# Kernel optimization log

Measured on AMD Instinct MI355X. Metric: run time of the kernel, lower is better.

Reference implementation:

```python
import jax, jax.numpy as jnp
import numpy as np

S, B, H = 2048, 2, 2048
NH = 16
HD = H // NH
SCALE = HD ** -0.5


def setup_inputs() -> dict:
    key = jax.random.key(0)
    ks = jax.random.split(key, 5)
    sigma = 0.02
    return {
        "x": jax.random.normal(ks[0], (S, B, H), dtype=jnp.float32),
        "wq": jax.random.normal(ks[1], (H, H), dtype=jnp.float32) * sigma,
        "wk": jax.random.normal(ks[2], (H, H), dtype=jnp.float32) * sigma,
        "wv": jax.random.normal(ks[3], (H, H), dtype=jnp.float32) * sigma,
        "wo": jax.random.normal(ks[4], (H, H), dtype=jnp.float32) * sigma,
    }


def reference(x, wq, wk, wv, wo):
    # x: [s, b, h]; F.linear(x, W) == x @ W.T
    q = x @ wq.T
    k = x @ wk.T
    v = x @ wv.T
    s, b, _ = q.shape
    # [s, b, h] -> [b, nh, s, hd]
    def split_heads(t):
        return t.reshape(s, b, NH, HD).transpose(1, 2, 0, 3)
    q, k, v = split_heads(q), split_heads(k), split_heads(v)
    scores = jnp.einsum("bhqd,bhkd->bhqk", q, k) * SCALE
    attn = jax.nn.softmax(scores.astype(jnp.float32), axis=-1).astype(q.dtype)
    out = jnp.einsum("bhqk,bhkd->bhqd", attn, v)
    # [b, nh, s, hd] -> [s, b, h]
    out = out.transpose(2, 0, 1, 3).reshape(s, b, NH * HD)
    return out @ wo.T
```

## Files before the change

### kernel.cpp

```cpp
#include <hip/hip_runtime.h>

typedef __bf16 bf16;
typedef __bf16 bf16x8 __attribute__((ext_vector_type(8)));
typedef float f32x4 __attribute__((ext_vector_type(4)));
typedef float f32x16 __attribute__((ext_vector_type(16)));
typedef unsigned int uint;
typedef uint uint2v __attribute__((ext_vector_type(2)));

#define GLOAD16(g, l)                                                        \
  __builtin_amdgcn_global_load_lds(                                          \
      (const __attribute__((address_space(1))) void*)(g),                    \
      (__attribute__((address_space(3))) void*)(l), 16, 0, 0)

__device__ inline uint pack_bf16(float a, float b) {
  union { bf16 h[2]; uint u; } x;
  x.h[0] = (bf16)a; x.h[1] = (bf16)b;
  return x.u;
}

__global__ void cast_f32_to_bf16(const float* __restrict__ in,
                                 bf16* __restrict__ out, int n8, float scale) {
  int i = blockIdx.x * blockDim.x + threadIdx.x;
  if (i >= n8) return;
  const float4* p = reinterpret_cast<const float4*>(in) + (size_t)i * 2;
  float4 a = p[0], b = p[1];
  bf16x8 o;
  o[0] = (bf16)(a.x * scale); o[1] = (bf16)(a.y * scale);
  o[2] = (bf16)(a.z * scale); o[3] = (bf16)(a.w * scale);
  o[4] = (bf16)(b.x * scale); o[5] = (bf16)(b.y * scale);
  o[6] = (bf16)(b.z * scale); o[7] = (bf16)(b.w * scale);
  *reinterpret_cast<bf16x8*>(out + (size_t)i * 8) = o;
}

template <typename OT>
__global__ __launch_bounds__(512, 2) void gemm_nt_256(
    const bf16* __restrict__ A, const bf16* __restrict__ B, OT* __restrict__ C,
    int K, int lda, int ldb, int ldc, long bsB, long bsC, long cSplit) {
  extern __shared__ char sh[];
  const int t = threadIdx.x;
  const int w = t >> 6, lane = t & 63;
  const int l15 = lane & 15, l4 = lane >> 4;
  const int wr = w >> 1, wc = w & 1;
  const int gx = gridDim.x, gy = gridDim.y;
  const int nwg = gx * gy;
  const int bid = blockIdx.y * gx + blockIdx.x;
  const int fid = (bid & 7) * (nwg >> 3) + (bid >> 3);
  const int by = fid / gx, bx = fid - by * gx;
  const int m0 = by * 256;
  const int n0 = bx * 128;
  const bf16* Bg = B + (size_t)blockIdx.z * bsB;
  OT* Cg = C + (size_t)blockIdx.z * bsC + ((n0 & 2048) ? cSplit : 0);

  int sRow[4], sCol[4];
#pragma unroll
  for (int i = 0; i < 4; i++) {
    int sB_ = (i * 512 + t) * 16;
    int row = sB_ >> 7;
    int ge = (sB_ ^ ((row & 7) << 4)) >> 1;
    sRow[i] = ge >> 6;
    sCol[i] = ge & 63;
  }

  const int NT = K >> 6;
  f32x4 acc[4][4] = {};

  auto stage = [&](int tt) {
    char* dst = sh + (size_t)(tt % 3) * 49152;
    const int k0 = tt * 64;
#pragma unroll
    for (int i = 0; i < 4; i++)
      GLOAD16(A + (size_t)(m0 + sRow[i]) * lda + k0 + sCol[i],
              dst + (i * 512 + w * 64) * 16);
#pragma unroll
    for (int i = 0; i < 2; i++)
      GLOAD16(Bg + (size_t)(n0 + sRow[i]) * ldb + k0 + sCol[i],
              dst + 32768 + (i * 512 + w * 64) * 16);
  };

  stage(0);
  stage(1);
  for (int tt = 0; tt < NT; ++tt) {
    if (tt < NT - 1)
      asm volatile("s_waitcnt vmcnt(6)" ::: "memory");
    else
      asm volatile("s_waitcnt vmcnt(0)" ::: "memory");
    __builtin_amdgcn_s_barrier();

    const char* Ab = sh + (size_t)(tt % 3) * 49152;
    const char* Bb = Ab + 32768;
    bf16x8 bfr[4][2];
#pragma unroll
    for (int n = 0; n < 4; n++)
#pragma unroll
      for (int kk = 0; kk < 2; kk++) {
        int row = wc * 64 + n * 16 + l15;
        int off = (row * 128 + kk * 64 + l4 * 16) ^ ((row & 7) << 4);
        bfr[n][kk] = *reinterpret_cast<const bf16x8*>(Bb + off);
      }
    bf16x8 af0[2][2];
#pragma unroll
    for (int m = 0; m < 2; m++)
#pragma unroll
      for (int kk = 0; kk < 2; kk++) {
        int row = wr * 64 + m * 16 + l15;
        int off = (row * 128 + kk * 64 + l4 * 16) ^ ((row & 7) << 4);
        af0[m][kk] = *reinterpret_cast<const bf16x8*>(Ab + off);
      }
    __builtin_amdgcn_s_setprio(1);
#pragma unroll
    for (int m = 0; m < 2; m++)
#pragma unroll
      for (int n = 0; n < 4; n++)
#pragma unroll
        for (int kk = 0; kk < 2; kk++)
          acc[m][n] = __builtin_amdgcn_mfma_f32_16x16x32_bf16(
              af0[m][kk], bfr[n][kk], acc[m][n], 0, 0, 0);
    __builtin_amdgcn_s_setprio(0);

    if (tt + 2 < NT) stage(tt + 2);

    bf16x8 af1[2][2];
#pragma unroll
    for (int m = 0; m < 2; m++)
#pragma unroll
      for (int kk = 0; kk < 2; kk++) {
        int row = wr * 64 + (2 + m) * 16 + l15;
        int off = (row * 128 + kk * 64 + l4 * 16) ^ ((row & 7) << 4);
        af1[m][kk] = *reinterpret_cast<const bf16x8*>(Ab + off);
      }
    __builtin_amdgcn_s_setprio(1);
#pragma unroll
    for (int m = 0; m < 2; m++)
#pragma unroll
      for (int n = 0; n < 4; n++)
#pragma unroll
        for (int kk = 0; kk < 2; kk++)
          acc[2 + m][n] = __builtin_amdgcn_mfma_f32_16x16x32_bf16(
              af1[m][kk], bfr[n][kk], acc[2 + m][n], 0, 0, 0);
    __builtin_amdgcn_s_setprio(0);
  }

#pragma unroll
  for (int m = 0; m < 4; m++)
#pragma unroll
    for (int n = 0; n < 4; n++)
#pragma unroll
      for (int j = 0; j < 4; j++) {
        int row = m0 + wr * 64 + m * 16 + l4 * 4 + j;
        int col = n0 + wc * 64 + n * 16 + l15;
        Cg[(size_t)row * ldc + col] = (OT)acc[m][n][j];
      }
}

__global__ __launch_bounds__(512, 2) void attn_fwd(
    const bf16* __restrict__ Q, const bf16* __restrict__ Kb,
    const bf16* __restrict__ Vt, bf16* __restrict__ O) {
  extern __shared__ char ash[];
  const int t = threadIdx.x, w = t >> 6, lane = t & 63;
  const int l31 = lane & 31, half = lane >> 5;
  const int bh = blockIdx.x;
  const int b = bh >> 4, h = bh & 15;
  const int sq0 = blockIdx.y * 256 + w * 32;
  const size_t hoff = (size_t)h * 128;
  const size_t bO = (size_t)b * 2048 + hoff;

  bf16x8 qf[8];
  {
    const bf16* qp = Q + ((size_t)(sq0 + l31) * 2 + b) * 2048 + hoff + half * 8;
#pragma unroll
    for (int dc = 0; dc < 8; dc++)
      qf[dc] = *reinterpret_cast<const bf16x8*>(qp + dc * 16);
  }

  const bf16* kp[2];
  const bf16* vp[2];
#pragma unroll
  for (int i = 0; i < 2; i++) {
    int s = i * 512 + t;
    int row = s >> 4, g = s & 15;
    int lg = g ^ (row & 15);
    kp[i] = Kb + ((size_t)row * 2 + b) * 2048 + hoff + lg * 8;
    int d = row * 2 + (lg >> 3);
    vp[i] = Vt + (bO + d) * 2048 + (lg & 7) * 8;
  }

  auto stage = [&](int slot, int sk0) {
    char* Kd = ash + (size_t)slot * 32768;
    char* Vd = Kd + 16384;
#pragma unroll
    for (int i = 0; i < 2; i++)
      GLOAD16(kp[i] + (size_t)sk0 * 4096, Kd + (i * 512 + w * 64) * 16);
#pragma unroll
    for (int i = 0; i < 2; i++)
      GLOAD16(vp[i] + sk0, Vd + (i * 512 + w * 64) * 16);
  };

  f32x16 acc_o[4] = {};
  float m_run = -3e38f, l_run = 0.f;

  stage(0, 0);
  stage(1, 64);

  for (int it = 0; it < 32; ++it) {
    if (it < 31)
      asm volatile("s_waitcnt vmcnt(4)" ::: "memory");
    else
      asm volatile("s_waitcnt vmcnt(0)" ::: "memory");
    __builtin_amdgcn_s_barrier();

    const char* ksb = ash + (size_t)(it % 3) * 32768;
    const char* vsb = ksb + 16384;

    f32x16 sc[2] = {};
    __builtin_amdgcn_s_setprio(1);
#pragma unroll
    for (int dc = 0; dc < 8; dc++) {
      int kx = ((dc * 2 + half) ^ (l31 & 15)) << 4;
#pragma unroll
      for (int kt = 0; kt < 2; kt++) {
        int kB = ((kt * 32 + l31) << 8) + kx;
        bf16x8 kf = *reinterpret_cast<const bf16x8*>(ksb + kB);
        sc[kt] = __builtin_amdgcn_mfma_f32_32x32x16_bf16(kf, qf[dc], sc[kt], 0, 0, 0);
      }
    }
    __builtin_amdgcn_s_setprio(0);

    if (it + 2 < 32) stage((it + 2) % 3, (it + 2) * 64);

    float red[8];
#pragma unroll
    for (int r = 0; r < 8; r++)
      red[r] = fmaxf(fmaxf(sc[0][r], sc[0][r + 8]),
                     fmaxf(sc[1][r], sc[1][r + 8]));
#pragma unroll
    for (int s = 4; s >= 1; s >>= 1)
#pragma unroll
      for (int r = 0; r < s; r++) red[r] = fmaxf(red[r], red[r + s]);
    float pmax = fmaxf(red[0], __shfl_xor(red[0], 32));

    if (!__all(pmax - m_run <= 11.0f)) {
      float mn = fmaxf(m_run, pmax);
      float f = exp2f(m_run - mn);
      m_run = mn;
      l_run *= f;
#pragma unroll
      for (int idx = 0; idx < 16; idx++) {
        float fr = __shfl(f, (idx & 3) + 8 * (idx >> 2) + half * 4);
#pragma unroll
        for (int dcb = 0; dcb < 4; dcb++) acc_o[dcb][idx] *= fr;
      }
    }

#pragma unroll
    for (int kt = 0; kt < 2; kt++)
#pragma unroll
      for (int r = 0; r < 16; r++) sc[kt][r] = exp2f(sc[kt][r] - m_run);
#pragma unroll
    for (int r = 0; r < 8; r++)
      red[r] = (sc[0][r] + sc[0][r + 8]) + (sc[1][r] + sc[1][r + 8]);
#pragma unroll
    for (int s = 4; s >= 1; s >>= 1)
#pragma unroll
      for (int r = 0; r < s; r++) red[r] += red[r + s];
    l_run += red[0] + __shfl_xor(red[0], 32);

    uint pa[4][4];
#pragma unroll
    for (int skc = 0; skc < 4; skc++) {
      int kt = skc >> 1, s8 = (skc & 1) * 8;
      uint pk01 = pack_bf16(sc[kt][s8 + 0], sc[kt][s8 + 1]);
      uint pk23 = pack_bf16(sc[kt][s8 + 2], sc[kt][s8 + 3]);
      uint pk45 = pack_bf16(sc[kt][s8 + 4], sc[kt][s8 + 5]);
      uint pk67 = pack_bf16(sc[kt][s8 + 6], sc[kt][s8 + 7]);
      uint2v r02 = __builtin_amdgcn_permlane32_swap(pk01, pk45, false, false);
      uint2v r13 = __builtin_amdgcn_permlane32_swap(pk23, pk67, false, false);
      pa[skc][0] = r02[0];
      pa[skc][1] = r13[0];
      pa[skc][2] = r02[1];
      pa[skc][3] = r13[1];
    }

    __builtin_amdgcn_s_setprio(1);
#pragma unroll
    for (int dcb = 0; dcb < 4; dcb++) {
      int rp = dcb * 16 + (l31 >> 1);
      int pbit = (l31 & 1) << 3;
#pragma unroll
      for (int skc = 0; skc < 4; skc++) {
        int vB = (rp << 8) + (((pbit + skc * 2 + half) ^ (l31 >> 1)) << 4);
        bf16x8 vf = *reinterpret_cast<const bf16x8*>(vsb + vB);
        union { uint u[4]; bf16x8 v; } af;
        af.u[0] = pa[skc][0]; af.u[1] = pa[skc][1];
        af.u[2] = pa[skc][2]; af.u[3] = pa[skc][3];
        acc_o[dcb] = __builtin_amdgcn_mfma_f32_32x32x16_bf16(
            af.v, vf, acc_o[dcb], 0, 0, 0);
      }
    }
    __builtin_amdgcn_s_setprio(0);
  }

  float inv = 1.0f / l_run;
#pragma unroll
  for (int idx = 0; idx < 16; idx++) {
    int sr = (idx & 3) + 8 * (idx >> 2) + half * 4;
    float invr = __shfl(inv, sr);
    bf16* op = O + ((size_t)(sq0 + sr) * 2 + b) * 2048 + hoff + l31;
#pragma unroll
    for (int dcb = 0; dcb < 4; dcb++)
      op[dcb * 32] = (bf16)(acc_o[dcb][idx] * invr);
  }
}

extern "C" void kernel_launch(void* const* d_in, const int* in_sizes, int n_in,
                              void* d_out, int out_size, void* d_ws,
                              size_t ws_size, hipStream_t stream) {
  (void)in_sizes; (void)n_in; (void)out_size; (void)ws_size;
  const float* x  = (const float*)d_in[0];
  const float* wq = (const float*)d_in[1];
  const float* wk = (const float*)d_in[2];
  const float* wv = (const float*)d_in[3];
  const float* wo = (const float*)d_in[4];
  float* out = (float*)d_out;
  char* ws = (char*)d_ws;
  bf16* xb   = (bf16*)(ws);
  bf16* qb   = (bf16*)(ws + (1u << 24));
  bf16* kb   = (bf16*)(ws + (2u << 24));
  bf16* vt   = (bf16*)(ws + (3u << 24));
  bf16* wb   = (bf16*)(ws + (4u << 24));
  bf16* wqk  = vt;
  bf16* attn = xb;
  const float SCALE = 0.08838834764831845f * 1.4426950408889634f;
  const int SMEM = 3 * 49152;
  const int SMEM_A = 3 * 32768;
  const long CSPLIT = (long)(kb - qb) - 2048;

  hipFuncSetAttribute((const void*)gemm_nt_256<bf16>,
                      hipFuncAttributeMaxDynamicSharedMemorySize, SMEM);
  hipFuncSetAttribute((const void*)gemm_nt_256<float>,
                      hipFuncAttributeMaxDynamicSharedMemorySize, SMEM);
  hipFuncSetAttribute((const void*)attn_fwd,
                      hipFuncAttributeMaxDynamicSharedMemorySize, SMEM_A);

  cast_f32_to_bf16<<<4096, 256, 0, stream>>>(x, xb, 8388608 / 8, 1.0f);

  cast_f32_to_bf16<<<2048, 256, 0, stream>>>(wq, wqk, 4194304 / 8, SCALE);
  cast_f32_to_bf16<<<2048, 256, 0, stream>>>(wk, wqk + 4194304, 4194304 / 8, 1.0f);
  dim3 gqk(32, 16, 1);
  gemm_nt_256<bf16><<<gqk, 512, SMEM, stream>>>(xb, wqk, qb, 2048, 2048, 2048,
                                                2048, 0, 0, CSPLIT);

  cast_f32_to_bf16<<<2048, 256, 0, stream>>>(wv, wb, 4194304 / 8, 1.0f);
  dim3 g2(16, 8, 2);
  gemm_nt_256<bf16><<<g2, 512, SMEM, stream>>>(wb, xb, vt, 2048, 2048, 4096, 2048,
                                               2048L, 4194304L, 0);

  dim3 ga(32, 8);
  attn_fwd<<<ga, 512, SMEM_A, stream>>>(qb, kb, vt, attn);

  cast_f32_to_bf16<<<2048, 256, 0, stream>>>(wo, wb, 4194304 / 8, 1.0f);
  dim3 g1(16, 16, 1);
  gemm_nt_256<float><<<g1, 512, SMEM, stream>>>(attn, wb, out, 2048, 2048, 2048,
                                                2048, 0, 0, 0);
}
```

Measured before the change: 271.5 us.

## Fuse input casts into one kernel and software-pipeline LDS loads in attention

Replaces four separate f32-to-bf16 cast launches (x, wq, wk, wv) with a single cast4 kernel that picks its source and destination by index range, which cuts launch overhead and the gaps between launches. In the attention inner loop, the K and V fragments are now loaded from LDS into register groups ahead of the MFMAs that use them, so several groups are in flight while the previous group's MFMAs run. This hides LDS latency behind matrix math but raises VGPR pressure, which could lower occupancy or cause spills.

```diff
diff --git a/kernel.cpp b/kernel.cpp
--- a/kernel.cpp
+++ b/kernel.cpp
@@ -30,6 +30,35 @@
   o[4] = (bf16)(b.x * scale); o[5] = (bf16)(b.y * scale);
   o[6] = (bf16)(b.z * scale); o[7] = (bf16)(b.w * scale);
   *reinterpret_cast<bf16x8*>(out + (size_t)i * 8) = o;
+}
+
+__global__ void cast4(const float* __restrict__ x, const float* __restrict__ wq,
+                      const float* __restrict__ wk, const float* __restrict__ wv,
+                      bf16* __restrict__ xb, bf16* __restrict__ wqk,
+                      bf16* __restrict__ wvb, float qscale) {
+  int i = blockIdx.x * blockDim.x + threadIdx.x;
+  const float* src;
+  bf16* dst;
+  float s = 1.0f;
+  int j;
+  if (i < 1048576) {
+    src = x; dst = xb; j = i;
+  } else {
+    int k = i - 1048576;
+    int r = k >> 19;
+    j = k & 524287;
+    src = r == 0 ? wq : r == 1 ? wk : wv;
+    dst = r == 0 ? wqk : r == 1 ? wqk + 4194304 : wvb;
+    s = r == 0 ? qscale : 1.0f;
+  }
+  const float4* p = reinterpret_cast<const float4*>(src) + (size_t)j * 2;
+  float4 a = p[0], b = p[1];
+  bf16x8 o;
+  o[0] = (bf16)(a.x * s); o[1] = (bf16)(a.y * s);
+  o[2] = (bf16)(a.z * s); o[3] = (bf16)(a.w * s);
+  o[4] = (bf16)(b.x * s); o[5] = (bf16)(b.y * s);
+  o[6] = (bf16)(b.z * s); o[7] = (bf16)(b.w * s);
+  *reinterpret_cast<bf16x8*>(dst + (size_t)j * 8) = o;
 }
 
 template <typename OT>
@@ -212,17 +241,35 @@
     const char* vsb = ksb + 16384;
 
     f32x16 sc[2] = {};
+    bf16x8 ka[4], kb_[4], kc[4];
+    auto loadK = [&](bf16x8 (&dst)[4], int g) {
+#pragma unroll
+      for (int j = 0; j < 2; j++) {
+        int dc = g * 2 + j;
+        int kx = ((dc * 2 + half) ^ (l31 & 15)) << 4;
+        dst[j * 2 + 0] = *reinterpret_cast<const bf16x8*>(ksb + (l31 << 8) + kx);
+        dst[j * 2 + 1] =
+            *reinterpret_cast<const bf16x8*>(ksb + ((32 + l31) << 8) + kx);
+      }
+    };
+    auto mfmaK = [&](bf16x8 (&kf)[4], int g) {
+#pragma unroll
+      for (int j = 0; j < 2; j++) {
+        sc[0] = __builtin_amdgcn_mfma_f32_32x32x16_bf16(kf[j * 2 + 0],
+                                                        qf[g * 2 + j], sc[0], 0, 0, 0);
+        sc[1] = __builtin_amdgcn_mfma_f32_32x32x16_bf16(kf[j * 2 + 1],
+                                                        qf[g * 2 + j], sc[1], 0, 0, 0);
+      }
+    };
+    loadK(ka, 0);
+    loadK(kb_, 1);
+    loadK(kc, 2);
     __builtin_amdgcn_s_setprio(1);
-#pragma unroll
-    for (int dc = 0; dc < 8; dc++) {
-      int kx = ((dc * 2 + half) ^ (l31 & 15)) << 4;
-#pragma unroll
-      for (int kt = 0; kt < 2; kt++) {
-        int kB = ((kt * 32 + l31) << 8) + kx;
-        bf16x8 kf = *reinterpret_cast<const bf16x8*>(ksb + kB);
-        sc[kt] = __builtin_amdgcn_mfma_f32_32x32x16_bf16(kf, qf[dc], sc[kt], 0, 0, 0);
-      }
-    }
+    mfmaK(ka, 0);
+    loadK(ka, 3);
+    mfmaK(kb_, 1);
+    mfmaK(kc, 2);
+    mfmaK(ka, 3);
     __builtin_amdgcn_s_setprio(0);
 
     if (it + 2 < 32) stage((it + 2) % 3, (it + 2) * 64);
@@ -263,6 +310,19 @@
 #pragma unroll
       for (int r = 0; r < s; r++) red[r] += red[r + s];
     l_run += red[0] + __shfl_xor(red[0], 32);
+
+    bf16x8 va[4], vb[4], vc[4];
+    auto loadV = [&](bf16x8 (&dst)[4], int dcb) {
+      int rp = dcb * 16 + (l31 >> 1);
+      int pbit = (l31 & 1) << 3;
+#pragma unroll
+      for (int skc = 0; skc < 4; skc++)
+        dst[skc] = *reinterpret_cast<const bf16x8*>(
+            vsb + (rp << 8) + (((pbit + skc * 2 + half) ^ (l31 >> 1)) << 4));
+    };
+    loadV(va, 0);
+    loadV(vb, 1);
+    loadV(vc, 2);
 
     uint pa[4][4];
 #pragma unroll
@@ -280,22 +340,22 @@
       pa[skc][3] = r13[1];
     }
 
-    __builtin_amdgcn_s_setprio(1);
-#pragma unroll
-    for (int dcb = 0; dcb < 4; dcb++) {
-      int rp = dcb * 16 + (l31 >> 1);
-      int pbit = (l31 & 1) << 3;
+    auto mfmaV = [&](bf16x8 (&vf)[4], int dcb) {
 #pragma unroll
       for (int skc = 0; skc < 4; skc++) {
-        int vB = (rp << 8) + (((pbit + skc * 2 + half) ^ (l31 >> 1)) << 4);
-        bf16x8 vf = *reinterpret_cast<const bf16x8*>(vsb + vB);
         union { uint u[4]; bf16x8 v; } af;
         af.u[0] = pa[skc][0]; af.u[1] = pa[skc][1];
         af.u[2] = pa[skc][2]; af.u[3] = pa[skc][3];
         acc_o[dcb] = __builtin_amdgcn_mfma_f32_32x32x16_bf16(
-            af.v, vf, acc_o[dcb], 0, 0, 0);
-      }
-    }
+            af.v, vf[skc], acc_o[dcb], 0, 0, 0);
+      }
+    };
+    __builtin_amdgcn_s_setprio(1);
+    mfmaV(va, 0);
+    loadV(va, 3);
+    mfmaV(vb, 1);
+    mfmaV(vc, 2);
+    mfmaV(va, 3);
     __builtin_amdgcn_s_setprio(0);
   }
 
@@ -341,15 +401,12 @@
   hipFuncSetAttribute((const void*)attn_fwd,
                       hipFuncAttributeMaxDynamicSharedMemorySize, SMEM_A);
 
-  cast_f32_to_bf16<<<4096, 256, 0, stream>>>(x, xb, 8388608 / 8, 1.0f);
-
-  cast_f32_to_bf16<<<2048, 256, 0, stream>>>(wq, wqk, 4194304 / 8, SCALE);
-  cast_f32_to_bf16<<<2048, 256, 0, stream>>>(wk, wqk + 4194304, 4194304 / 8, 1.0f);
+  cast4<<<10240, 256, 0, stream>>>(x, wq, wk, wv, xb, wqk, wb, SCALE);
+
   dim3 gqk(32, 16, 1);
   gemm_nt_256<bf16><<<gqk, 512, SMEM, stream>>>(xb, wqk, qb, 2048, 2048, 2048,
                                                 2048, 0, 0, CSPLIT);
 
-  cast_f32_to_bf16<<<2048, 256, 0, stream>>>(wv, wb, 4194304 / 8, 1.0f);
   dim3 g2(16, 8, 2);
   gemm_nt_256<bf16><<<g2, 512, SMEM, stream>>>(wb, xb, vt, 2048, 2048, 4096, 2048,
                                                2048L, 4194304L, 0);
```

Result: faster. 264.4 us (-2.6%).
